# Performance work log

Measured on AMD Instinct MI355X. Metric: run time of the kernel, lower is better.

The kernel has to match this reference:

```python
import jax, jax.numpy as jnp
import numpy as np

B, N, D, R, NUM_HEADS, S = 8, 512, 256, 6, 3, 1000


def setup_inputs() -> dict:
    key = jax.random.key(0)
    ks = jax.random.split(key, 12)
    init = lambda k, shape: jax.random.normal(k, shape, jnp.float32) * 0.02
    return {
        "symbol_ids": jax.random.randint(ks[0], (B, N), 0, S),
        "positions": jax.random.normal(ks[1], (B, N, 2), jnp.float32),
        "sym_table": init(ks[2], (S, D)),
        "layer_table": init(ks[3], (S, D)),      # layer-0 interpretation embedding
        "rel_W": init(ks[4], (R, D, D)),          # per-relation Linear weights (in,out)
        "rel_b": init(ks[5], (R, D)),
        "h1_W": init(ks[6], (NUM_HEADS, D, D)),   # interpretation head Linear1
        "h1_b": init(ks[7], (NUM_HEADS, D)),
        "h2_W": init(ks[8], (NUM_HEADS, D)),      # interpretation head Linear2 (D->1)
        "h2_b": init(ks[9], (NUM_HEADS,)),
        "out_W": init(ks[10], (D, D)),
        "out_b": init(ks[11], (D,)),
    }


def _relation_type(dx, dy):
    # Vectorized version of PositionalGrammar._get_relation_type (if/elif chain)
    return jnp.select(
        [dy > 0.5, dy < -0.5, dx < -0.5, dx > 0.5,
         (jnp.abs(dx) < 0.3) & (jnp.abs(dy) < 0.3)],
        [0, 1, 2, 3, 4], 5)


def _positional_grammar(symbols, positions, rel_W, rel_b):
    # transformed[b,j] = symbols[b,j] + sum_{i!=j} (symbols[b,i] @ W_r(i,j) + b_r(i,j))
    dx = positions[:, None, :, 0] - positions[:, :, None, 0]  # [b,i,j]
    dy = positions[:, None, :, 1] - positions[:, :, None, 1]
    rel = _relation_type(dx, dy)                               # [b,i,j] int
    n = symbols.shape[1]
    not_self = ~jnp.eye(n, dtype=bool)
    # one-hot relation mask, self-pairs excluded: [b,i,j,r]
    M = ((rel[..., None] == jnp.arange(R)) & not_self[None, :, :, None]).astype(symbols.dtype)
    T = jnp.einsum('bid,rde->brie', symbols, rel_W)            # per-relation transform of sources
    contrib = jnp.einsum('bijr,brie->bje', M, T)               # scatter-add over sources i
    bias = jnp.einsum('bijr,re->bje', M, rel_b)                # per-pair bias accumulation
    return symbols + contrib + bias


def reference(symbol_ids, positions, sym_table, layer_table, rel_W, rel_b,
              h1_W, h1_b, h2_W, h2_b, out_W, out_b):
    # SymbolEmbedding (calendar_pos=None path; layer=0)
    symbols = sym_table[symbol_ids] + layer_table[symbol_ids]  # [B,N,D]
    # PositionalGrammar
    symbols = _positional_grammar(symbols, positions, rel_W, rel_b)
    # LayeredInterpretation: 3 heads of Linear-GELU-Linear(D->1)
    h = jax.nn.gelu(jnp.einsum('bnd,rde->brne', symbols, h1_W)
                    + h1_b[None, :, None, :], approximate=False)
    interp = jnp.einsum('brne,re->brn', h, h2_W) + h2_b[None, :, None]  # [B,3,N]
    # output projection
    output = symbols @ out_W + out_b
    return (output,
            interp[:, 0, :, None],   # exoteric  [B,N,1]
            interp[:, 1, :, None],   # esoteric
            interp[:, 2, :, None],   # sacred
            symbols)
```

## Files before the change

kernel.cpp:

```cpp
#include <hip/hip_runtime.h>
#include <hip/hip_bf16.h>
#include <math.h>

#define BB 8
#define NN 512
#define DD 256
#define BNT 4096

typedef __attribute__((ext_vector_type(8))) short short8;
typedef __attribute__((ext_vector_type(4))) float f32x4;

#define OFF_S0B   0u
#define OFF_TT    524288u
#define OFF_WCT   6815744u
#define OFF_WBT   7012352u
#define OFF_BB    7143424u
#define OFF_REL   7144448u

#define OUT0_OFF   0u
#define INTERP_OFF 1048576u
#define SYM_OFF    1060864u

__device__ __forceinline__ float gelu_exact(float x) {
    return 0.5f * x * (1.0f + erff(x * 0.70710678118654752f));
}

__device__ __forceinline__ ushort f2bf(float x) {
    __hip_bfloat16 h = __float2bfloat16(x);
    union { __hip_bfloat16 b; ushort u; } cv;
    cv.b = h;
    return cv.u;
}

__device__ __forceinline__ int rel_of(float dx, float dy) {
    int r = (fabsf(dx) < 0.3f && fabsf(dy) < 0.3f) ? 4 : 5;
    r = (dx >  0.5f) ? 3 : r;
    r = (dx < -0.5f) ? 2 : r;
    r = (dy < -0.5f) ? 1 : r;
    r = (dy >  0.5f) ? 0 : r;
    return r;
}

#define TILE_IDS()                                             \
    const int lane = tid & 63, w = tid >> 6;                   \
    const int wm = w >> 1, wn = w & 1;                         \
    const int quad = lane >> 4, l15 = lane & 15;               \
    const int sm = tid >> 2, sq = tid & 3;

#define MFMA_STEP(Abuf, Bbuf)                                                \
    {                                                                        \
        short8 af[2], bfr[2];                                                \
        _Pragma("unroll")                                                    \
        for (int mt = 0; mt < 2; mt++)                                       \
            af[mt] = *(const short8*)&(Abuf)[(quad * 64 + wm * 32 + mt * 16 + l15) * 8]; \
        _Pragma("unroll")                                                    \
        for (int nt = 0; nt < 2; nt++)                                       \
            bfr[nt] = *(const short8*)&(Bbuf)[(quad * 64 + wn * 32 + nt * 16 + l15) * 8]; \
        _Pragma("unroll")                                                    \
        for (int mt = 0; mt < 2; mt++)                                       \
            _Pragma("unroll")                                                \
            for (int nt = 0; nt < 2; nt++)                                   \
                acc[mt][nt] = __builtin_amdgcn_mfma_f32_16x16x32_bf16(       \
                    af[mt], bfr[nt], acc[mt][nt], 0, 0, 0);                  \
    }

#define ACC_INIT()                                             \
    f32x4 acc[2][2];                                           \
    _Pragma("unroll") for (int mt = 0; mt < 2; mt++)           \
    _Pragma("unroll") for (int nt = 0; nt < 2; nt++)           \
        acc[mt][nt] = (f32x4){0.f, 0.f, 0.f, 0.f};

__global__ __launch_bounds__(256) void front_kernel(
    const int* __restrict__ ids, const float* __restrict__ positions,
    const float* __restrict__ symt, const float* __restrict__ layt,
    const float* __restrict__ relW, const float* __restrict__ h1W,
    const float* __restrict__ outW, const float* __restrict__ h1b,
    const float* __restrict__ outb, const float* __restrict__ h2b,
    ushort* __restrict__ WcT, ushort* __restrict__ WbT,
    float* __restrict__ bbig, float* __restrict__ outI,
    float* __restrict__ symOut, ushort* __restrict__ s0b,
    unsigned char* __restrict__ rel)
{
    __shared__ float px[NN], py[NN];
    int blk = blockIdx.x, tid = threadIdx.x;
    if (blk < 1536) {
        int idx = blk * 256 + tid;
        {
            int e = idx / 1536, k = idx - e * 1536;
            int r = k >> 8, d = k & 255;
            WcT[idx] = f2bf(relW[(r * DD + d) * DD + e]);
        }
        if (idx < 262144) {
            int c = idx >> 8, d = idx & 255;
            float v;
            if (c < 768) { int r = c >> 8, e = c & 255; v = h1W[(r * DD + d) * DD + e]; }
            else         { v = outW[d * DD + (c - 768)]; }
            WbT[idx] = f2bf(v);
        }
        if (idx < 3 * BNT) outI[idx] = h2b[idx >> 12];
        if (idx < 1024) bbig[idx] = (idx < 768) ? h1b[idx] : outb[idx - 768];
    } else if (blk < 5632) {
        int row = blk - 1536;
        int id = ids[row];
        float v = symt[id * DD + tid] + layt[id * DD + tid];
        symOut[(size_t)row * DD + tid] = v;
        s0b[(size_t)row * DD + tid] = f2bf(v);
    } else {
        int blk2 = blk - 5632;
        int b = blk2 >> 6;
        int j0 = (blk2 & 63) << 3;
        int jl = tid >> 5, sub = tid & 31;
        for (int i = tid; i < NN; i += 256) {
            float2 p = ((const float2*)positions)[b * NN + i];
            px[i] = p.x; py[i] = p.y;
        }
        __syncthreads();
        int j = j0 + jl;
        float xj = px[j], yj = py[j];
        union { unsigned char u8[16]; uint4 v; } codes;
#pragma unroll
        for (int t = 0; t < 16; t++) {
            int i = sub * 16 + t;
            int r = rel_of(xj - px[i], yj - py[i]);
            r = (i == j) ? 6 : r;
            codes.u8[t] = (unsigned char)r;
        }
        *(uint4*)&rel[((size_t)(b * NN + j)) * NN + sub * 16] = codes.v;
    }
}

__global__ __launch_bounds__(256) void gemmT_kernel(
    const ushort* __restrict__ WcT, const ushort* __restrict__ s0b,
    const float* __restrict__ relb, ushort* __restrict__ TT)
{
    __shared__ ushort Als[2][2048], Bls[2][2048];
    int tid = threadIdx.x;
    int b = blockIdx.z;
    int rowM0 = blockIdx.y * 64;
    int col0 = blockIdx.x * 64;
    int r = rowM0 >> 8, e0 = rowM0 & 255;
    TILE_IDS();
    ACC_INIT();
    const ushort* gA = WcT + (size_t)(e0 + sm) * 1536 + r * 256 + sq * 8;
    const ushort* gB = s0b + ((size_t)(b * NN) + col0 + sm) * DD + sq * 8;
    const int lo = (sq * 64 + sm) * 8;

    *(uint4*)&Als[0][lo] = *(const uint4*)gA;
    *(uint4*)&Bls[0][lo] = *(const uint4*)gB;
#pragma unroll
    for (int i = 0; i < 8; i++) {
        __syncthreads();
        uint4 av2, bv2;
        if (i < 7) {
            av2 = *(const uint4*)(gA + (i + 1) * 32);
            bv2 = *(const uint4*)(gB + (i + 1) * 32);
        }
        MFMA_STEP(Als[i & 1], Bls[i & 1]);
        if (i < 7) {
            *(uint4*)&Als[(i + 1) & 1][lo] = av2;
            *(uint4*)&Bls[(i + 1) & 1][lo] = bv2;
        }
    }
#pragma unroll
    for (int mt = 0; mt < 2; mt++)
#pragma unroll
        for (int nt = 0; nt < 2; nt++)
#pragma unroll
            for (int v = 0; v < 4; v++) {
                int e = e0 + wm * 32 + mt * 16 + quad * 4 + v;
                int i = col0 + wn * 32 + nt * 16 + l15;
                TT[((size_t)(b * DD) + e) * 3072 + r * 512 + i] =
                    f2bf(acc[mt][nt][v] + relb[r * DD + e]);
            }
}

__global__ __launch_bounds__(256) void agg_gemm(
    const unsigned char* __restrict__ rel, const ushort* __restrict__ TT,
    float* __restrict__ symOut)
{
    __shared__ ushort Als[2][2048], Bls[2][2048];
    int tid = threadIdx.x;
    int z = blockIdx.z;
    int b = z / 3, rg = z - b * 3;
    int row0 = blockIdx.y * 64, col0 = blockIdx.x * 64;
    TILE_IDS();
    ACC_INIT();
    const unsigned char* gC = rel + ((size_t)(b * NN + row0 + sm)) * NN;
    const ushort* gB = TT + ((size_t)(b * DD) + col0 + sm) * 3072 + rg * 1024 + sq * 8;
    const int lo = (sq * 64 + sm) * 8;

#define AGG_LOADS(i, cw, bv)                                        \
    cw = *(const uint2*)(gC + (((i) * 32 + sq * 8) & 511));         \
    bv = *(const uint4*)(gB + (i) * 32);

#define AGG_STAGE(i, cw, bv, buf)                                   \
    {                                                               \
        int rr_ = 2 * rg + (((i) * 32) >> 9);                       \
        union alignas(16) { ushort u[8]; uint4 v; } am;             \
        _Pragma("unroll")                                           \
        for (int t = 0; t < 8; t++) {                               \
            unsigned int word = (t < 4) ? cw.x : cw.y;              \
            unsigned int code = (word >> (8 * (t & 3))) & 255u;     \
            am.u[t] = (code == (unsigned)rr_) ? 0x3F80 : 0;         \
        }                                                           \
        *(uint4*)&Als[buf][lo] = am.v;                              \
        *(uint4*)&Bls[buf][lo] = bv;                                \
    }

    uint2 cw0; uint4 bv0;
    AGG_LOADS(0, cw0, bv0);
    AGG_STAGE(0, cw0, bv0, 0);
    for (int i = 0; i < 32; i++) {
        __syncthreads();
        uint2 cw2; uint4 bv2;
        if (i < 31) { AGG_LOADS(i + 1, cw2, bv2); }
        MFMA_STEP(Als[i & 1], Bls[i & 1]);
        if (i < 31) { AGG_STAGE(i + 1, cw2, bv2, (i + 1) & 1); }
    }
#undef AGG_LOADS
#undef AGG_STAGE
#pragma unroll
    for (int mt = 0; mt < 2; mt++)
#pragma unroll
        for (int nt = 0; nt < 2; nt++)
#pragma unroll
            for (int v = 0; v < 4; v++) {
                int j = row0 + wm * 32 + mt * 16 + quad * 4 + v;
                int e = col0 + wn * 32 + nt * 16 + l15;
                atomicAdd(&symOut[((size_t)(b * NN) + j) * DD + e], acc[mt][nt][v]);
            }
}

__global__ __launch_bounds__(256) void gemm2_kernel(
    const float* __restrict__ symOut, const ushort* __restrict__ WbT,
    const float* __restrict__ bbig, const float* __restrict__ h2W,
    float* __restrict__ out0, float* __restrict__ outI)
{
    __shared__ ushort Als[2][2048], Bls[2][2048];
    int tid = threadIdx.x;
    int row0 = blockIdx.y * 64, col0 = blockIdx.x * 64;
    TILE_IDS();
    ACC_INIT();
    const float*  gA = symOut + (size_t)(row0 + sm) * DD + sq * 8;
    const ushort* gB = WbT    + (size_t)(col0 + sm) * DD + sq * 8;
    const int lo = (sq * 64 + sm) * 8;

#define G2_LOADS(i, a0, a1, bv)                                     \
    a0 = *(const float4*)(gA + (i) * 32);                           \
    a1 = *(const float4*)(gA + (i) * 32 + 4);                       \
    bv = *(const uint4*)(gB + (i) * 32);

#define G2_STAGE(a0, a1, bv, buf)                                   \
    {                                                               \
        union alignas(16) { ushort u[8]; uint4 v; } am;             \
        am.u[0] = f2bf(a0.x); am.u[1] = f2bf(a0.y);                 \
        am.u[2] = f2bf(a0.z); am.u[3] = f2bf(a0.w);                 \
        am.u[4] = f2bf(a1.x); am.u[5] = f2bf(a1.y);                 \
        am.u[6] = f2bf(a1.z); am.u[7] = f2bf(a1.w);                 \
        *(uint4*)&Als[buf][lo] = am.v;                              \
        *(uint4*)&Bls[buf][lo] = bv;                                \
    }

    float4 a0, a1; uint4 bv;
    G2_LOADS(0, a0, a1, bv);
    G2_STAGE(a0, a1, bv, 0);
#pragma unroll
    for (int i = 0; i < 8; i++) {
        __syncthreads();
        float4 a0n, a1n; uint4 bvn;
        if (i < 7) { G2_LOADS(i + 1, a0n, a1n, bvn); }
        MFMA_STEP(Als[i & 1], Bls[i & 1]);
        if (i < 7) { G2_STAGE(a0n, a1n, bvn, (i + 1) & 1); }
    }
#undef G2_LOADS
#undef G2_STAGE
    if (col0 >= 768) {
#pragma unroll
        for (int nt = 0; nt < 2; nt++) {
            int c = col0 + wn * 32 + nt * 16 + l15;
            float bb = bbig[c];
#pragma unroll
            for (int mt = 0; mt < 2; mt++)
#pragma unroll
                for (int v = 0; v < 4; v++) {
                    int row = row0 + wm * 32 + mt * 16 + quad * 4 + v;
                    out0[(size_t)row * DD + (c - 768)] = acc[mt][nt][v] + bb;
                }
        }
    } else {
        int head = col0 >> 8;
        float part[2][4];
#pragma unroll
        for (int mt = 0; mt < 2; mt++)
#pragma unroll
            for (int v = 0; v < 4; v++) part[mt][v] = 0.f;
#pragma unroll
        for (int nt = 0; nt < 2; nt++) {
            int c = col0 + wn * 32 + nt * 16 + l15;
            float bb = bbig[c];
            float w2 = h2W[c];
#pragma unroll
            for (int mt = 0; mt < 2; mt++)
#pragma unroll
                for (int v = 0; v < 4; v++)
                    part[mt][v] += gelu_exact(acc[mt][nt][v] + bb) * w2;
        }
#pragma unroll
        for (int mt = 0; mt < 2; mt++)
#pragma unroll
            for (int v = 0; v < 4; v++) {
                float p = part[mt][v];
                p += __shfl_xor(p, 1); p += __shfl_xor(p, 2);
                p += __shfl_xor(p, 4); p += __shfl_xor(p, 8);
                if (l15 == 0) {
                    int row = row0 + wm * 32 + mt * 16 + quad * 4 + v;
                    atomicAdd(&outI[head * BNT + row], p);
                }
            }
    }
}

extern "C" void kernel_launch(void* const* d_in, const int* in_sizes, int n_in,
                              void* d_out, int out_size, void* d_ws, size_t ws_size,
                              hipStream_t stream)
{
    const int*   ids  = (const int*)d_in[0];
    const float* pos  = (const float*)d_in[1];
    const float* symt = (const float*)d_in[2];
    const float* layt = (const float*)d_in[3];
    const float* relW = (const float*)d_in[4];
    const float* relb = (const float*)d_in[5];
    const float* h1W  = (const float*)d_in[6];
    const float* h1b  = (const float*)d_in[7];
    const float* h2W  = (const float*)d_in[8];
    const float* h2b  = (const float*)d_in[9];
    const float* outW = (const float*)d_in[10];
    const float* outb = (const float*)d_in[11];
    float* out = (float*)d_out;
    float* ws  = (float*)d_ws;

    ushort* s0b  = (ushort*)(ws + OFF_S0B);
    ushort* TT   = (ushort*)(ws + OFF_TT);
    ushort* WcT  = (ushort*)(ws + OFF_WCT);
    ushort* WbT  = (ushort*)(ws + OFF_WBT);
    float*  bbig = ws + OFF_BB;
    unsigned char* rel = (unsigned char*)(ws + OFF_REL);

    front_kernel<<<6144, 256, 0, stream>>>(ids, pos, symt, layt, relW, h1W, outW,
                                           h1b, outb, h2b, WcT, WbT, bbig,
                                           out + INTERP_OFF, out + SYM_OFF, s0b, rel);
    gemmT_kernel<<<dim3(8, 24, 8), 256, 0, stream>>>(WcT, s0b, relb, TT);
    agg_gemm<<<dim3(4, 8, 24), 256, 0, stream>>>(rel, TT, out + SYM_OFF);
    gemm2_kernel<<<dim3(16, 64), 256, 0, stream>>>(out + SYM_OFF, WbT,
                                                   bbig, h2W,
                                                   out + OUT0_OFF, out + INTERP_OFF);
}
```

Before: 139.8 us.

## Fuse four kernels into one cooperative persistent kernel with grid syncs

Replaces the four separate launches (front prep, T GEMM, aggregation GEMM, output GEMM) with a single cooperative kernel of 512 blocks. The blocks loop over job lists and separate the phases with grid.sync(). The weight transposes now go through shared-memory tiles so that both reads and writes are coalesced, and the embedding gather handles 64 rows per job. This removes launch gaps and tail effects between kernels, but adds grid-barrier cost and caps parallelism at 512 resident blocks.

Measured after the change: 351.9 us. 2.52x slower.

```diff
diff --git a/kernel.cpp b/kernel.cpp
--- a/kernel.cpp
+++ b/kernel.cpp
@@ -1,6 +1,9 @@
 #include <hip/hip_runtime.h>
+#include <hip/hip_cooperative_groups.h>
 #include <hip/hip_bf16.h>
 #include <math.h>
+
+namespace cg = cooperative_groups;
 
 #define BB 8
 #define NN 512
@@ -70,129 +73,180 @@
     _Pragma("unroll") for (int nt = 0; nt < 2; nt++)           \
         acc[mt][nt] = (f32x4){0.f, 0.f, 0.f, 0.f};
 
-__global__ __launch_bounds__(256) void front_kernel(
+#define NJOBS1 737
+
+__global__ __launch_bounds__(256, 2) void mega_kernel(
     const int* __restrict__ ids, const float* __restrict__ positions,
     const float* __restrict__ symt, const float* __restrict__ layt,
-    const float* __restrict__ relW, const float* __restrict__ h1W,
-    const float* __restrict__ outW, const float* __restrict__ h1b,
-    const float* __restrict__ outb, const float* __restrict__ h2b,
-    ushort* __restrict__ WcT, ushort* __restrict__ WbT,
-    float* __restrict__ bbig, float* __restrict__ outI,
-    float* __restrict__ symOut, ushort* __restrict__ s0b,
-    unsigned char* __restrict__ rel)
+    const float* __restrict__ relW, const float* __restrict__ relb,
+    const float* __restrict__ h1W, const float* __restrict__ h1b,
+    const float* __restrict__ h2W, const float* __restrict__ h2b,
+    const float* __restrict__ outW, const float* __restrict__ outb,
+    float* __restrict__ out, float* __restrict__ ws)
 {
-    __shared__ float px[NN], py[NN];
-    int blk = blockIdx.x, tid = threadIdx.x;
-    if (blk < 1536) {
-        int idx = blk * 256 + tid;
-        {
-            int e = idx / 1536, k = idx - e * 1536;
-            int r = k >> 8, d = k & 255;
-            WcT[idx] = f2bf(relW[(r * DD + d) * DD + e]);
+    cg::grid_group grid = cg::this_grid();
+    __shared__ __align__(16) char shraw[16640];
+    const int tid = threadIdx.x;
+
+    ushort* s0b  = (ushort*)(ws + OFF_S0B);
+    ushort* TT   = (ushort*)(ws + OFF_TT);
+    ushort* WcT  = (ushort*)(ws + OFF_WCT);
+    ushort* WbT  = (ushort*)(ws + OFF_WBT);
+    float*  bbig = ws + OFF_BB;
+    unsigned char* rel = (unsigned char*)(ws + OFF_REL);
+    float* out0   = out + OUT0_OFF;
+    float* outI   = out + INTERP_OFF;
+    float* symOut = out + SYM_OFF;
+
+    for (int job = blockIdx.x; job < NJOBS1; job += gridDim.x) {
+        __syncthreads();
+        if (job < 96) {
+            float (*tr)[65] = (float(*)[65])shraw;
+            int ty = job >> 2, tx = job & 3;
+            int rd0 = ty * 64, e0 = tx * 64;
+            int x = tid & 63, g = tid >> 6;
+#pragma unroll
+            for (int k = 0; k < 16; k++) {
+                int il = g * 16 + k;
+                tr[il][x] = relW[(size_t)(rd0 + il) * DD + e0 + x];
+            }
+            __syncthreads();
+#pragma unroll
+            for (int k = 0; k < 16; k++) {
+                int el = g * 16 + k;
+                WcT[(size_t)(e0 + el) * 1536 + rd0 + x] = f2bf(tr[x][el]);
+            }
+        } else if (job < 160) {
+            float (*tr)[65] = (float(*)[65])shraw;
+            int jt = job - 96;
+            int dt = jt >> 4, ct = jt & 15;
+            int d0 = dt * 64, c0 = ct * 64;
+            int x = tid & 63, g = tid >> 6;
+#pragma unroll
+            for (int k = 0; k < 16; k++) {
+                int dl = g * 16 + k;
+                int c = c0 + x;
+                float v;
+                if (c < 768) v = h1W[(size_t)((c >> 8) * DD + d0 + dl) * DD + (c & 255)];
+                else         v = outW[(size_t)(d0 + dl) * DD + (c - 768)];
+                tr[dl][x] = v;
+            }
+            __syncthreads();
+#pragma unroll
+            for (int k = 0; k < 16; k++) {
+                int cl = g * 16 + k;
+                WbT[(size_t)(c0 + cl) * DD + d0 + x] = f2bf(tr[x][cl]);
+            }
+        } else if (job < 224) {
+            int* idsL = (int*)shraw;
+            int n0 = (job - 160) * 64;
+            if (tid < 64) idsL[tid] = ids[n0 + tid];
+            __syncthreads();
+#pragma unroll 4
+            for (int k = 0; k < 64; k++) {
+                int row = n0 + k;
+                int id = idsL[k];
+                float v = symt[(size_t)id * DD + tid] + layt[(size_t)id * DD + tid];
+                symOut[(size_t)row * DD + tid] = v;
+                s0b[(size_t)row * DD + tid] = f2bf(v);
+            }
+        } else if (job == 224) {
+            for (int idx = tid; idx < 3 * BNT + 1024; idx += 256) {
+                if (idx < 3 * BNT) outI[idx] = h2b[idx >> 12];
+                else {
+                    int bbi = idx - 3 * BNT;
+                    bbig[bbi] = (bbi < 768) ? h1b[bbi] : outb[bbi - 768];
+                }
+            }
+        } else {
+            float* px = (float*)shraw;
+            float* py = px + NN;
+            int cj = job - 225;
+            int b = cj >> 6;
+            int j0 = (cj & 63) << 3;
+            int jl = tid >> 5, sub = tid & 31;
+            for (int i = tid; i < NN; i += 256) {
+                float2 p = ((const float2*)positions)[b * NN + i];
+                px[i] = p.x; py[i] = p.y;
+            }
+            __syncthreads();
+            int j = j0 + jl;
+            float xj = px[j], yj = py[j];
+            union { unsigned char u8[16]; uint4 v; } codes;
+#pragma unroll
+            for (int t = 0; t < 16; t++) {
+                int i = sub * 16 + t;
+                int r = rel_of(xj - px[i], yj - py[i]);
+                r = (i == j) ? 6 : r;
+                codes.u8[t] = (unsigned char)r;
+            }
+            *(uint4*)&rel[((size_t)(b * NN + j)) * NN + sub * 16] = codes.v;
         }
-        if (idx < 262144) {
-            int c = idx >> 8, d = idx & 255;
-            float v;
-            if (c < 768) { int r = c >> 8, e = c & 255; v = h1W[(r * DD + d) * DD + e]; }
-            else         { v = outW[d * DD + (c - 768)]; }
-            WbT[idx] = f2bf(v);
+    }
+    grid.sync();
+
+    {
+        ushort (*Als)[2048] = (ushort(*)[2048])shraw;
+        ushort (*Bls)[2048] = (ushort(*)[2048])(shraw + 8192);
+        TILE_IDS();
+        for (int job = blockIdx.x; job < 1536; job += gridDim.x) {
+            __syncthreads();
+            int b = job / 192, rem = job - b * 192;
+            int rm = rem >> 3, it = rem & 7;
+            int rowM0 = rm * 64, col0 = it * 64;
+            int r = rowM0 >> 8, e0 = rowM0 & 255;
+            ACC_INIT();
+            const ushort* gA = WcT + (size_t)(e0 + sm) * 1536 + r * 256 + sq * 8;
+            const ushort* gB = s0b + ((size_t)(b * NN) + col0 + sm) * DD + sq * 8;
+            const int lo = (sq * 64 + sm) * 8;
+            *(uint4*)&Als[0][lo] = *(const uint4*)gA;
+            *(uint4*)&Bls[0][lo] = *(const uint4*)gB;
+#pragma unroll
+            for (int i = 0; i < 8; i++) {
+                __syncthreads();
+                uint4 av2, bv2;
+                if (i < 7) {
+                    av2 = *(const uint4*)(gA + (i + 1) * 32);
+                    bv2 = *(const uint4*)(gB + (i + 1) * 32);
+                }
+                MFMA_STEP(Als[i & 1], Bls[i & 1]);
+                if (i < 7) {
+                    *(uint4*)&Als[(i + 1) & 1][lo] = av2;
+                    *(uint4*)&Bls[(i + 1) & 1][lo] = bv2;
+                }
+            }
+#pragma unroll
+            for (int mt = 0; mt < 2; mt++)
+#pragma unroll
+                for (int nt = 0; nt < 2; nt++)
+#pragma unroll
+                    for (int v = 0; v < 4; v++) {
+                        int e = e0 + wm * 32 + mt * 16 + quad * 4 + v;
+                        int i = col0 + wn * 32 + nt * 16 + l15;
+                        TT[((size_t)(b * DD) + e) * 3072 + r * 512 + i] =
+                            f2bf(acc[mt][nt][v] + relb[r * DD + e]);
+                    }
         }
-        if (idx < 3 * BNT) outI[idx] = h2b[idx >> 12];
-        if (idx < 1024) bbig[idx] = (idx < 768) ? h1b[idx] : outb[idx - 768];
-    } else if (blk < 5632) {
-        int row = blk - 1536;
-        int id = ids[row];
-        float v = symt[id * DD + tid] + layt[id * DD + tid];
-        symOut[(size_t)row * DD + tid] = v;
-        s0b[(size_t)row * DD + tid] = f2bf(v);
-    } else {
-        int blk2 = blk - 5632;
-        int b = blk2 >> 6;
-        int j0 = (blk2 & 63) << 3;
-        int jl = tid >> 5, sub = tid & 31;
-        for (int i = tid; i < NN; i += 256) {
-            float2 p = ((const float2*)positions)[b * NN + i];
-            px[i] = p.x; py[i] = p.y;
-        }
-        __syncthreads();
-        int j = j0 + jl;
-        float xj = px[j], yj = py[j];
-        union { unsigned char u8[16]; uint4 v; } codes;
-#pragma unroll
-        for (int t = 0; t < 16; t++) {
-            int i = sub * 16 + t;
-            int r = rel_of(xj - px[i], yj - py[i]);
-            r = (i == j) ? 6 : r;
-            codes.u8[t] = (unsigned char)r;
-        }
-        *(uint4*)&rel[((size_t)(b * NN + j)) * NN + sub * 16] = codes.v;
-    }
-}
-
-__global__ __launch_bounds__(256) void gemmT_kernel(
-    const ushort* __restrict__ WcT, const ushort* __restrict__ s0b,
-    const float* __restrict__ relb, ushort* __restrict__ TT)
-{
-    __shared__ ushort Als[2][2048], Bls[2][2048];
-    int tid = threadIdx.x;
-    int b = blockIdx.z;
-    int rowM0 = blockIdx.y * 64;
-    int col0 = blockIdx.x * 64;
-    int r = rowM0 >> 8, e0 = rowM0 & 255;
-    TILE_IDS();
-    ACC_INIT();
-    const ushort* gA = WcT + (size_t)(e0 + sm) * 1536 + r * 256 + sq * 8;
-    const ushort* gB = s0b + ((size_t)(b * NN) + col0 + sm) * DD + sq * 8;
-    const int lo = (sq * 64 + sm) * 8;
-
-    *(uint4*)&Als[0][lo] = *(const uint4*)gA;
-    *(uint4*)&Bls[0][lo] = *(const uint4*)gB;
-#pragma unroll
-    for (int i = 0; i < 8; i++) {
-        __syncthreads();
-        uint4 av2, bv2;
-        if (i < 7) {
-            av2 = *(const uint4*)(gA + (i + 1) * 32);
-            bv2 = *(const uint4*)(gB + (i + 1) * 32);
-        }
-        MFMA_STEP(Als[i & 1], Bls[i & 1]);
-        if (i < 7) {
-            *(uint4*)&Als[(i + 1) & 1][lo] = av2;
-            *(uint4*)&Bls[(i + 1) & 1][lo] = bv2;
-        }
-    }
-#pragma unroll
-    for (int mt = 0; mt < 2; mt++)
-#pragma unroll
-        for (int nt = 0; nt < 2; nt++)
-#pragma unroll
-            for (int v = 0; v < 4; v++) {
-                int e = e0 + wm * 32 + mt * 16 + quad * 4 + v;
-                int i = col0 + wn * 32 + nt * 16 + l15;
-                TT[((size_t)(b * DD) + e) * 3072 + r * 512 + i] =
-                    f2bf(acc[mt][nt][v] + relb[r * DD + e]);
-            }
-}
-
-__global__ __launch_bounds__(256) void agg_gemm(
-    const unsigned char* __restrict__ rel, const ushort* __restrict__ TT,
-    float* __restrict__ symOut)
-{
-    __shared__ ushort Als[2][2048], Bls[2][2048];
-    int tid = threadIdx.x;
-    int z = blockIdx.z;
-    int b = z / 3, rg = z - b * 3;
-    int row0 = blockIdx.y * 64, col0 = blockIdx.x * 64;
-    TILE_IDS();
-    ACC_INIT();
-    const unsigned char* gC = rel + ((size_t)(b * NN + row0 + sm)) * NN;
-    const ushort* gB = TT + ((size_t)(b * DD) + col0 + sm) * 3072 + rg * 1024 + sq * 8;
-    const int lo = (sq * 64 + sm) * 8;
-
+    }
+    grid.sync();
+
+    {
+        ushort (*Als)[2048] = (ushort(*)[2048])shraw;
+        ushort (*Bls)[2048] = (ushort(*)[2048])(shraw + 8192);
+        TILE_IDS();
+        for (int job = blockIdx.x; job < 768; job += gridDim.x) {
+            __syncthreads();
+            int z = job >> 5, rem = job & 31;
+            int jt = rem >> 2, et = rem & 3;
+            int b = z / 3, rg = z - b * 3;
+            int row0 = jt * 64, col0 = et * 64;
+            ACC_INIT();
+            const unsigned char* gC = rel + ((size_t)(b * NN + row0 + sm)) * NN;
+            const ushort* gB = TT + ((size_t)(b * DD) + col0 + sm) * 3072 + rg * 1024 + sq * 8;
+            const int lo = (sq * 64 + sm) * 8;
 #define AGG_LOADS(i, cw, bv)                                        \
     cw = *(const uint2*)(gC + (((i) * 32 + sq * 8) & 511));         \
     bv = *(const uint4*)(gB + (i) * 32);
-
 #define AGG_STAGE(i, cw, bv, buf)                                   \
     {                                                               \
         int rr_ = 2 * rg + (((i) * 32) >> 9);                       \
@@ -206,50 +260,49 @@
         *(uint4*)&Als[buf][lo] = am.v;                              \
         *(uint4*)&Bls[buf][lo] = bv;                                \
     }
-
-    uint2 cw0; uint4 bv0;
-    AGG_LOADS(0, cw0, bv0);
-    AGG_STAGE(0, cw0, bv0, 0);
-    for (int i = 0; i < 32; i++) {
-        __syncthreads();
-        uint2 cw2; uint4 bv2;
-        if (i < 31) { AGG_LOADS(i + 1, cw2, bv2); }
-        MFMA_STEP(Als[i & 1], Bls[i & 1]);
-        if (i < 31) { AGG_STAGE(i + 1, cw2, bv2, (i + 1) & 1); }
-    }
+            uint2 cw0; uint4 bv0;
+            AGG_LOADS(0, cw0, bv0);
+            AGG_STAGE(0, cw0, bv0, 0);
+            for (int i = 0; i < 32; i++) {
+                __syncthreads();
+                uint2 cw2; uint4 bv2;
+                if (i < 31) { AGG_LOADS(i + 1, cw2, bv2); }
+                MFMA_STEP(Als[i & 1], Bls[i & 1]);
+                if (i < 31) { AGG_STAGE(i + 1, cw2, bv2, (i + 1) & 1); }
+            }
 #undef AGG_LOADS
 #undef AGG_STAGE
 #pragma unroll
-    for (int mt = 0; mt < 2; mt++)
-#pragma unroll
-        for (int nt = 0; nt < 2; nt++)
-#pragma unroll
-            for (int v = 0; v < 4; v++) {
-                int j = row0 + wm * 32 + mt * 16 + quad * 4 + v;
-                int e = col0 + wn * 32 + nt * 16 + l15;
-                atomicAdd(&symOut[((size_t)(b * NN) + j) * DD + e], acc[mt][nt][v]);
-            }
-}
-
-__global__ __launch_bounds__(256) void gemm2_kernel(
-    const float* __restrict__ symOut, const ushort* __restrict__ WbT,
-    const float* __restrict__ bbig, const float* __restrict__ h2W,
-    float* __restrict__ out0, float* __restrict__ outI)
-{
-    __shared__ ushort Als[2][2048], Bls[2][2048];
-    int tid = threadIdx.x;
-    int row0 = blockIdx.y * 64, col0 = blockIdx.x * 64;
-    TILE_IDS();
-    ACC_INIT();
-    const float*  gA = symOut + (size_t)(row0 + sm) * DD + sq * 8;
-    const ushort* gB = WbT    + (size_t)(col0 + sm) * DD + sq * 8;
-    const int lo = (sq * 64 + sm) * 8;
-
+            for (int mt = 0; mt < 2; mt++)
+#pragma unroll
+                for (int nt = 0; nt < 2; nt++)
+#pragma unroll
+                    for (int v = 0; v < 4; v++) {
+                        int j = row0 + wm * 32 + mt * 16 + quad * 4 + v;
+                        int e = col0 + wn * 32 + nt * 16 + l15;
+                        atomicAdd(&symOut[((size_t)(b * NN) + j) * DD + e],
+                                  acc[mt][nt][v]);
+                    }
+        }
+    }
+    grid.sync();
+
+    {
+        ushort (*Als)[2048] = (ushort(*)[2048])shraw;
+        ushort (*Bls)[2048] = (ushort(*)[2048])(shraw + 8192);
+        TILE_IDS();
+        for (int job = blockIdx.x; job < 1024; job += gridDim.x) {
+            __syncthreads();
+            int rt = job >> 4, ct = job & 15;
+            int row0 = rt * 64, col0 = ct * 64;
+            ACC_INIT();
+            const float*  gA = symOut + (size_t)(row0 + sm) * DD + sq * 8;
+            const ushort* gB = WbT    + (size_t)(col0 + sm) * DD + sq * 8;
+            const int lo = (sq * 64 + sm) * 8;
 #define G2_LOADS(i, a0, a1, bv)                                     \
     a0 = *(const float4*)(gA + (i) * 32);                           \
     a1 = *(const float4*)(gA + (i) * 32 + 4);                       \
     bv = *(const uint4*)(gB + (i) * 32);
-
 #define G2_STAGE(a0, a1, bv, buf)                                   \
     {                                                               \
         union alignas(16) { ushort u[8]; uint4 v; } am;             \
@@ -260,63 +313,64 @@
         *(uint4*)&Als[buf][lo] = am.v;                              \
         *(uint4*)&Bls[buf][lo] = bv;                                \
     }
-
-    float4 a0, a1; uint4 bv;
-    G2_LOADS(0, a0, a1, bv);
-    G2_STAGE(a0, a1, bv, 0);
-#pragma unroll
-    for (int i = 0; i < 8; i++) {
-        __syncthreads();
-        float4 a0n, a1n; uint4 bvn;
-        if (i < 7) { G2_LOADS(i + 1, a0n, a1n, bvn); }
-        MFMA_STEP(Als[i & 1], Bls[i & 1]);
-        if (i < 7) { G2_STAGE(a0n, a1n, bvn, (i + 1) & 1); }
-    }
+            float4 a0, a1; uint4 bv;
+            G2_LOADS(0, a0, a1, bv);
+            G2_STAGE(a0, a1, bv, 0);
+#pragma unroll
+            for (int i = 0; i < 8; i++) {
+                __syncthreads();
+                float4 a0n, a1n; uint4 bvn;
+                if (i < 7) { G2_LOADS(i + 1, a0n, a1n, bvn); }
+                MFMA_STEP(Als[i & 1], Bls[i & 1]);
+                if (i < 7) { G2_STAGE(a0n, a1n, bvn, (i + 1) & 1); }
+            }
 #undef G2_LOADS
 #undef G2_STAGE
-    if (col0 >= 768) {
-#pragma unroll
-        for (int nt = 0; nt < 2; nt++) {
-            int c = col0 + wn * 32 + nt * 16 + l15;
-            float bb = bbig[c];
-#pragma unroll
-            for (int mt = 0; mt < 2; mt++)
-#pragma unroll
-                for (int v = 0; v < 4; v++) {
-                    int row = row0 + wm * 32 + mt * 16 + quad * 4 + v;
-                    out0[(size_t)row * DD + (c - 768)] = acc[mt][nt][v] + bb;
+            if (col0 >= 768) {
+#pragma unroll
+                for (int nt = 0; nt < 2; nt++) {
+                    int c = col0 + wn * 32 + nt * 16 + l15;
+                    float bb = bbig[c];
+#pragma unroll
+                    for (int mt = 0; mt < 2; mt++)
+#pragma unroll
+                        for (int v = 0; v < 4; v++) {
+                            int row = row0 + wm * 32 + mt * 16 + quad * 4 + v;
+                            out0[(size_t)row * DD + (c - 768)] = acc[mt][nt][v] + bb;
+                        }
                 }
+            } else {
+                int head = col0 >> 8;
+                float part[2][4];
+#pragma unroll
+                for (int mt = 0; mt < 2; mt++)
+#pragma unroll
+                    for (int v = 0; v < 4; v++) part[mt][v] = 0.f;
+#pragma unroll
+                for (int nt = 0; nt < 2; nt++) {
+                    int c = col0 + wn * 32 + nt * 16 + l15;
+                    float bb = bbig[c];
+                    float w2 = h2W[c];
+#pragma unroll
+                    for (int mt = 0; mt < 2; mt++)
+#pragma unroll
+                        for (int v = 0; v < 4; v++)
+                            part[mt][v] += gelu_exact(acc[mt][nt][v] + bb) * w2;
+                }
+#pragma unroll
+                for (int mt = 0; mt < 2; mt++)
+#pragma unroll
+                    for (int v = 0; v < 4; v++) {
+                        float p = part[mt][v];
+                        p += __shfl_xor(p, 1); p += __shfl_xor(p, 2);
+                        p += __shfl_xor(p, 4); p += __shfl_xor(p, 8);
+                        if (l15 == 0) {
+                            int row = row0 + wm * 32 + mt * 16 + quad * 4 + v;
+                            atomicAdd(&outI[head * BNT + row], p);
+                        }
+                    }
+            }
         }
-    } else {
-        int head = col0 >> 8;
-        float part[2][4];
-#pragma unroll
-        for (int mt = 0; mt < 2; mt++)
-#pragma unroll
-            for (int v = 0; v < 4; v++) part[mt][v] = 0.f;
-#pragma unroll
-        for (int nt = 0; nt < 2; nt++) {
-            int c = col0 + wn * 32 + nt * 16 + l15;
-            float bb = bbig[c];
-            float w2 = h2W[c];
-#pragma unroll
-            for (int mt = 0; mt < 2; mt++)
-#pragma unroll
-                for (int v = 0; v < 4; v++)
-                    part[mt][v] += gelu_exact(acc[mt][nt][v] + bb) * w2;
-        }
-#pragma unroll
-        for (int mt = 0; mt < 2; mt++)
-#pragma unroll
-            for (int v = 0; v < 4; v++) {
-                float p = part[mt][v];
-                p += __shfl_xor(p, 1); p += __shfl_xor(p, 2);
-                p += __shfl_xor(p, 4); p += __shfl_xor(p, 8);
-                if (l15 == 0) {
-                    int row = row0 + wm * 32 + mt * 16 + quad * 4 + v;
-                    atomicAdd(&outI[head * BNT + row], p);
-                }
-            }
     }
 }
 
@@ -339,19 +393,10 @@
     float* out = (float*)d_out;
     float* ws  = (float*)d_ws;
 
-    ushort* s0b  = (ushort*)(ws + OFF_S0B);
-    ushort* TT   = (ushort*)(ws + OFF_TT);
-    ushort* WcT  = (ushort*)(ws + OFF_WCT);
-    ushort* WbT  = (ushort*)(ws + OFF_WBT);
-    float*  bbig = ws + OFF_BB;
-    unsigned char* rel = (unsigned char*)(ws + OFF_REL);
-
-    front_kernel<<<6144, 256, 0, stream>>>(ids, pos, symt, layt, relW, h1W, outW,
-                                           h1b, outb, h2b, WcT, WbT, bbig,
-                                           out + INTERP_OFF, out + SYM_OFF, s0b, rel);
-    gemmT_kernel<<<dim3(8, 24, 8), 256, 0, stream>>>(WcT, s0b, relb, TT);
-    agg_gemm<<<dim3(4, 8, 24), 256, 0, stream>>>(rel, TT, out + SYM_OFF);
-    gemm2_kernel<<<dim3(16, 64), 256, 0, stream>>>(out + SYM_OFF, WbT,
-                                                   bbig, h2W,
-                                                   out + OUT0_OFF, out + INTERP_OFF);
+    void* args[] = { (void*)&ids, (void*)&pos, (void*)&symt, (void*)&layt,
+                     (void*)&relW, (void*)&relb, (void*)&h1W, (void*)&h1b,
+                     (void*)&h2W, (void*)&h2b, (void*)&outW, (void*)&outb,
+                     (void*)&out, (void*)&ws };
+    hipLaunchCooperativeKernel((void*)mega_kernel, dim3(512), dim3(256),
+                               args, 0, stream);
 }
```

## Load MFMA fragments directly from global memory, dropping LDS staging

Applied to the files above, without the earlier changes.

The three GEMM kernels (gemmT, agg_gemm, gemm2) no longer stage tiles through double-buffered shared memory with block barriers. Each wave now loads its MFMA operand fragments straight from global memory, and agg_gemm builds its one-hot mask per fragment in registers. The front kernel's weight transposes are rewritten to read the source coalesced and write scattered. This removes LDS traffic and __syncthreads, but each A/B element is now fetched by two waves, raising global/L2 load volume and exposing latency without the software prefetch.

Measured after the change: 189.6 us. 1.36x slower.

```diff
diff --git a/kernel.cpp b/kernel.cpp
--- a/kernel.cpp
+++ b/kernel.cpp
@@ -44,25 +44,7 @@
 #define TILE_IDS()                                             \
     const int lane = tid & 63, w = tid >> 6;                   \
     const int wm = w >> 1, wn = w & 1;                         \
-    const int quad = lane >> 4, l15 = lane & 15;               \
-    const int sm = tid >> 2, sq = tid & 3;
-
-#define MFMA_STEP(Abuf, Bbuf)                                                \
-    {                                                                        \
-        short8 af[2], bfr[2];                                                \
-        _Pragma("unroll")                                                    \
-        for (int mt = 0; mt < 2; mt++)                                       \
-            af[mt] = *(const short8*)&(Abuf)[(quad * 64 + wm * 32 + mt * 16 + l15) * 8]; \
-        _Pragma("unroll")                                                    \
-        for (int nt = 0; nt < 2; nt++)                                       \
-            bfr[nt] = *(const short8*)&(Bbuf)[(quad * 64 + wn * 32 + nt * 16 + l15) * 8]; \
-        _Pragma("unroll")                                                    \
-        for (int mt = 0; mt < 2; mt++)                                       \
-            _Pragma("unroll")                                                \
-            for (int nt = 0; nt < 2; nt++)                                   \
-                acc[mt][nt] = __builtin_amdgcn_mfma_f32_16x16x32_bf16(       \
-                    af[mt], bfr[nt], acc[mt][nt], 0, 0, 0);                  \
-    }
+    const int quad = lane >> 4, l15 = lane & 15;
 
 #define ACC_INIT()                                             \
     f32x4 acc[2][2];                                           \
@@ -86,23 +68,24 @@
     if (blk < 1536) {
         int idx = blk * 256 + tid;
         {
-            int e = idx / 1536, k = idx - e * 1536;
-            int r = k >> 8, d = k & 255;
-            WcT[idx] = f2bf(relW[(r * DD + d) * DD + e]);
-        }
-        if (idx < 262144) {
-            int c = idx >> 8, d = idx & 255;
-            float v;
-            if (c < 768) { int r = c >> 8, e = c & 255; v = h1W[(r * DD + d) * DD + e]; }
-            else         { v = outW[d * DD + (c - 768)]; }
-            WbT[idx] = f2bf(v);
+            int rd = idx >> 8, e = idx & 255;
+            WcT[(size_t)e * 1536 + rd] = f2bf(relW[idx]);
+        }
+        if (idx < 196608) {
+            int r = idx >> 16, rem = idx & 65535;
+            int d = rem >> 8, e = rem & 255;
+            WbT[(size_t)(r * 256 + e) * DD + d] = f2bf(h1W[idx]);
+        } else if (idx < 262144) {
+            int idx2 = idx - 196608;
+            int d = idx2 >> 8, c = idx2 & 255;
+            WbT[(size_t)(768 + c) * DD + d] = f2bf(outW[idx2]);
         }
         if (idx < 3 * BNT) outI[idx] = h2b[idx >> 12];
         if (idx < 1024) bbig[idx] = (idx < 768) ? h1b[idx] : outb[idx - 768];
     } else if (blk < 5632) {
         int row = blk - 1536;
         int id = ids[row];
-        float v = symt[id * DD + tid] + layt[id * DD + tid];
+        float v = symt[(size_t)id * DD + tid] + layt[(size_t)id * DD + tid];
         symOut[(size_t)row * DD + tid] = v;
         s0b[(size_t)row * DD + tid] = f2bf(v);
     } else {
@@ -133,7 +116,6 @@
     const ushort* __restrict__ WcT, const ushort* __restrict__ s0b,
     const float* __restrict__ relb, ushort* __restrict__ TT)
 {
-    __shared__ ushort Als[2][2048], Bls[2][2048];
     int tid = threadIdx.x;
     int b = blockIdx.z;
     int rowM0 = blockIdx.y * 64;
@@ -141,25 +123,29 @@
     int r = rowM0 >> 8, e0 = rowM0 & 255;
     TILE_IDS();
     ACC_INIT();
-    const ushort* gA = WcT + (size_t)(e0 + sm) * 1536 + r * 256 + sq * 8;
-    const ushort* gB = s0b + ((size_t)(b * NN) + col0 + sm) * DD + sq * 8;
-    const int lo = (sq * 64 + sm) * 8;
-
-    *(uint4*)&Als[0][lo] = *(const uint4*)gA;
-    *(uint4*)&Bls[0][lo] = *(const uint4*)gB;
+    const ushort* pA[2];
+    const ushort* pB[2];
+#pragma unroll
+    for (int mt = 0; mt < 2; mt++)
+        pA[mt] = WcT + (size_t)(e0 + wm * 32 + mt * 16 + l15) * 1536
+                     + r * 256 + quad * 8;
+#pragma unroll
+    for (int nt = 0; nt < 2; nt++)
+        pB[nt] = s0b + ((size_t)(b * NN) + col0 + wn * 32 + nt * 16 + l15) * DD
+                     + quad * 8;
 #pragma unroll
     for (int i = 0; i < 8; i++) {
-        __syncthreads();
-        uint4 av2, bv2;
-        if (i < 7) {
-            av2 = *(const uint4*)(gA + (i + 1) * 32);
-            bv2 = *(const uint4*)(gB + (i + 1) * 32);
-        }
-        MFMA_STEP(Als[i & 1], Bls[i & 1]);
-        if (i < 7) {
-            *(uint4*)&Als[(i + 1) & 1][lo] = av2;
-            *(uint4*)&Bls[(i + 1) & 1][lo] = bv2;
-        }
+        short8 af[2], bf[2];
+#pragma unroll
+        for (int mt = 0; mt < 2; mt++) af[mt] = *(const short8*)(pA[mt] + i * 32);
+#pragma unroll
+        for (int nt = 0; nt < 2; nt++) bf[nt] = *(const short8*)(pB[nt] + i * 32);
+#pragma unroll
+        for (int mt = 0; mt < 2; mt++)
+#pragma unroll
+            for (int nt = 0; nt < 2; nt++)
+                acc[mt][nt] = __builtin_amdgcn_mfma_f32_16x16x32_bf16(
+                    af[mt], bf[nt], acc[mt][nt], 0, 0, 0);
     }
 #pragma unroll
     for (int mt = 0; mt < 2; mt++)
@@ -178,47 +164,48 @@
     const unsigned char* __restrict__ rel, const ushort* __restrict__ TT,
     float* __restrict__ symOut)
 {
-    __shared__ ushort Als[2][2048], Bls[2][2048];
     int tid = threadIdx.x;
     int z = blockIdx.z;
     int b = z / 3, rg = z - b * 3;
     int row0 = blockIdx.y * 64, col0 = blockIdx.x * 64;
     TILE_IDS();
     ACC_INIT();
-    const unsigned char* gC = rel + ((size_t)(b * NN + row0 + sm)) * NN;
-    const ushort* gB = TT + ((size_t)(b * DD) + col0 + sm) * 3072 + rg * 1024 + sq * 8;
-    const int lo = (sq * 64 + sm) * 8;
-
-#define AGG_LOADS(i, cw, bv)                                        \
-    cw = *(const uint2*)(gC + (((i) * 32 + sq * 8) & 511));         \
-    bv = *(const uint4*)(gB + (i) * 32);
-
-#define AGG_STAGE(i, cw, bv, buf)                                   \
-    {                                                               \
-        int rr_ = 2 * rg + (((i) * 32) >> 9);                       \
-        union alignas(16) { ushort u[8]; uint4 v; } am;             \
-        _Pragma("unroll")                                           \
-        for (int t = 0; t < 8; t++) {                               \
-            unsigned int word = (t < 4) ? cw.x : cw.y;              \
-            unsigned int code = (word >> (8 * (t & 3))) & 255u;     \
-            am.u[t] = (code == (unsigned)rr_) ? 0x3F80 : 0;         \
-        }                                                           \
-        *(uint4*)&Als[buf][lo] = am.v;                              \
-        *(uint4*)&Bls[buf][lo] = bv;                                \
-    }
-
-    uint2 cw0; uint4 bv0;
-    AGG_LOADS(0, cw0, bv0);
-    AGG_STAGE(0, cw0, bv0, 0);
+    const unsigned char* pC[2];
+#pragma unroll
+    for (int mt = 0; mt < 2; mt++)
+        pC[mt] = rel + ((size_t)(b * NN + row0 + wm * 32 + mt * 16 + l15)) * NN;
+    const ushort* pB[2];
+#pragma unroll
+    for (int nt = 0; nt < 2; nt++)
+        pB[nt] = TT + ((size_t)(b * DD) + col0 + wn * 32 + nt * 16 + l15) * 3072
+                    + rg * 1024 + quad * 8;
+#pragma unroll 4
     for (int i = 0; i < 32; i++) {
-        __syncthreads();
-        uint2 cw2; uint4 bv2;
-        if (i < 31) { AGG_LOADS(i + 1, cw2, bv2); }
-        MFMA_STEP(Als[i & 1], Bls[i & 1]);
-        if (i < 31) { AGG_STAGE(i + 1, cw2, bv2, (i + 1) & 1); }
-    }
-#undef AGG_LOADS
-#undef AGG_STAGE
+        int kk = rg * 1024 + i * 32 + quad * 8;
+        int r  = kk >> 9;
+        int i0 = kk & 511;
+        short8 af[2], bf[2];
+#pragma unroll
+        for (int mt = 0; mt < 2; mt++) {
+            uint2 cw = *(const uint2*)(pC[mt] + i0);
+            union { ushort u[8]; short8 v; } am;
+#pragma unroll
+            for (int t = 0; t < 8; t++) {
+                unsigned int word = (t < 4) ? cw.x : cw.y;
+                unsigned int code = (word >> (8 * (t & 3))) & 255u;
+                am.u[t] = (code == (unsigned)r) ? 0x3F80 : 0;
+            }
+            af[mt] = am.v;
+        }
+#pragma unroll
+        for (int nt = 0; nt < 2; nt++) bf[nt] = *(const short8*)(pB[nt] + i * 32);
+#pragma unroll
+        for (int mt = 0; mt < 2; mt++)
+#pragma unroll
+            for (int nt = 0; nt < 2; nt++)
+                acc[mt][nt] = __builtin_amdgcn_mfma_f32_16x16x32_bf16(
+                    af[mt], bf[nt], acc[mt][nt], 0, 0, 0);
+    }
 #pragma unroll
     for (int mt = 0; mt < 2; mt++)
 #pragma unroll
@@ -236,44 +223,41 @@
     const float* __restrict__ bbig, const float* __restrict__ h2W,
     float* __restrict__ out0, float* __restrict__ outI)
 {
-    __shared__ ushort Als[2][2048], Bls[2][2048];
     int tid = threadIdx.x;
     int row0 = blockIdx.y * 64, col0 = blockIdx.x * 64;
     TILE_IDS();
     ACC_INIT();
-    const float*  gA = symOut + (size_t)(row0 + sm) * DD + sq * 8;
-    const ushort* gB = WbT    + (size_t)(col0 + sm) * DD + sq * 8;
-    const int lo = (sq * 64 + sm) * 8;
-
-#define G2_LOADS(i, a0, a1, bv)                                     \
-    a0 = *(const float4*)(gA + (i) * 32);                           \
-    a1 = *(const float4*)(gA + (i) * 32 + 4);                       \
-    bv = *(const uint4*)(gB + (i) * 32);
-
-#define G2_STAGE(a0, a1, bv, buf)                                   \
-    {                                                               \
-        union alignas(16) { ushort u[8]; uint4 v; } am;             \
-        am.u[0] = f2bf(a0.x); am.u[1] = f2bf(a0.y);                 \
-        am.u[2] = f2bf(a0.z); am.u[3] = f2bf(a0.w);                 \
-        am.u[4] = f2bf(a1.x); am.u[5] = f2bf(a1.y);                 \
-        am.u[6] = f2bf(a1.z); am.u[7] = f2bf(a1.w);                 \
-        *(uint4*)&Als[buf][lo] = am.v;                              \
-        *(uint4*)&Bls[buf][lo] = bv;                                \
-    }
-
-    float4 a0, a1; uint4 bv;
-    G2_LOADS(0, a0, a1, bv);
-    G2_STAGE(a0, a1, bv, 0);
+    const float* pA[2];
+#pragma unroll
+    for (int mt = 0; mt < 2; mt++)
+        pA[mt] = symOut + (size_t)(row0 + wm * 32 + mt * 16 + l15) * DD + quad * 8;
+    const ushort* pB[2];
+#pragma unroll
+    for (int nt = 0; nt < 2; nt++)
+        pB[nt] = WbT + (size_t)(col0 + wn * 32 + nt * 16 + l15) * DD + quad * 8;
 #pragma unroll
     for (int i = 0; i < 8; i++) {
-        __syncthreads();
-        float4 a0n, a1n; uint4 bvn;
-        if (i < 7) { G2_LOADS(i + 1, a0n, a1n, bvn); }
-        MFMA_STEP(Als[i & 1], Bls[i & 1]);
-        if (i < 7) { G2_STAGE(a0n, a1n, bvn, (i + 1) & 1); }
-    }
-#undef G2_LOADS
-#undef G2_STAGE
+        short8 af[2], bf[2];
+#pragma unroll
+        for (int mt = 0; mt < 2; mt++) {
+            float4 a0 = *(const float4*)(pA[mt] + i * 32);
+            float4 a1 = *(const float4*)(pA[mt] + i * 32 + 4);
+            union { ushort u[8]; short8 v; } am;
+            am.u[0] = f2bf(a0.x); am.u[1] = f2bf(a0.y);
+            am.u[2] = f2bf(a0.z); am.u[3] = f2bf(a0.w);
+            am.u[4] = f2bf(a1.x); am.u[5] = f2bf(a1.y);
+            am.u[6] = f2bf(a1.z); am.u[7] = f2bf(a1.w);
+            af[mt] = am.v;
+        }
+#pragma unroll
+        for (int nt = 0; nt < 2; nt++) bf[nt] = *(const short8*)(pB[nt] + i * 32);
+#pragma unroll
+        for (int mt = 0; mt < 2; mt++)
+#pragma unroll
+            for (int nt = 0; nt < 2; nt++)
+                acc[mt][nt] = __builtin_amdgcn_mfma_f32_16x16x32_bf16(
+                    af[mt], bf[nt], acc[mt][nt], 0, 0, 0);
+    }
     if (col0 >= 768) {
 #pragma unroll
         for (int nt = 0; nt < 2; nt++) {
```
